# Kernel tuning notes

Hardware: AMD Instinct MI355X
Metric: run time of the kernel (lower is better)

The kernel has to match this reference:

```python
import jax, jax.numpy as jnp
import numpy as np
from jax import lax

BN_EPS = 1e-5


def fps(xyz, n_group):
    """Farthest point sampling. xyz: (B,N,3) -> indices (B,n_group)."""
    B, N, _ = xyz.shape

    def step(carry, _):
        dist, far = carry                                   # (B,N), (B,)
        c = jnp.take_along_axis(xyz, far[:, None, None], axis=1)  # (B,1,3)
        d = jnp.sum((xyz - c) ** 2, axis=-1)                # (B,N)
        dist = jnp.minimum(dist, d)
        return (dist, jnp.argmax(dist, axis=-1).astype(jnp.int32)), far

    init = (jnp.full((B, N), 1e10, xyz.dtype), jnp.zeros((B,), jnp.int32))
    _, idxs = lax.scan(step, init, None, length=n_group)
    return jnp.swapaxes(idxs, 0, 1)                         # (B,n_group)


def knn_point(k, xyz, center):
    """k nearest neighbors of each center in xyz. -> idx (B,G,k)."""
    # squared distances (B,G,N), expanded-cdist form
    d = (jnp.sum(center ** 2, -1)[:, :, None]
         + jnp.sum(xyz ** 2, -1)[:, None, :]
         - 2.0 * jnp.einsum('bgc,bnc->bgn', center, xyz))
    _, idx = lax.top_k(-d, k)                               # smallest distances
    return idx


def batchnorm(x, gamma, beta):
    """Training-mode BatchNorm1d over (M, n) per channel. x: (M,n,C)."""
    mu = jnp.mean(x, axis=(0, 1))
    var = jnp.var(x, axis=(0, 1))
    return (x - mu) * lax.rsqrt(var + BN_EPS) * gamma + beta


def encoder(pg, W1, b1, g1, be1, W2, b2, W3, b3, g2, be2, W4, b4):
    """PointNet encoder. pg: (B,G,n,3) -> (B,G,C)."""
    B, G, n, _ = pg.shape
    x = pg.reshape(B * G, n, 3)
    f = jnp.einsum('mnc,oc->mno', x, W1) + b1               # (M,n,128)
    f = jax.nn.relu(batchnorm(f, g1, be1))
    f = jnp.einsum('mnc,oc->mno', f, W2) + b2               # (M,n,256)
    fg = jnp.max(f, axis=1, keepdims=True)                  # (M,1,256)
    f = jnp.concatenate([jnp.broadcast_to(fg, f.shape), f], axis=-1)  # (M,n,512)
    f = jnp.einsum('mnc,oc->mno', f, W3) + b3               # (M,n,512)
    f = jax.nn.relu(batchnorm(f, g2, be2))
    f = jnp.einsum('mnc,oc->mno', f, W4) + b4               # (M,n,C)
    return jnp.max(f, axis=1).reshape(B, G, -1)


def setup_inputs() -> dict:
    key = jax.random.key(0)
    ks = jax.random.split(key, 8)
    C = 128
    xyz = jax.random.normal(ks[0], (16, 8192, 3), jnp.float32)
    s = 0.02
    return {
        'xyz': xyz,
        'W1': jax.random.normal(ks[1], (128, 3), jnp.float32) * s,
        'b1': jnp.zeros((128,), jnp.float32),
        'g1': jnp.ones((128,), jnp.float32),
        'be1': jnp.zeros((128,), jnp.float32),
        'W2': jax.random.normal(ks[2], (256, 128), jnp.float32) * s,
        'b2': jnp.zeros((256,), jnp.float32),
        'W3': jax.random.normal(ks[3], (512, 512), jnp.float32) * s,
        'b3': jnp.zeros((512,), jnp.float32),
        'g2': jnp.ones((512,), jnp.float32),
        'be2': jnp.zeros((512,), jnp.float32),
        'W4': jax.random.normal(ks[4], (C, 512), jnp.float32) * s,
        'b4': jnp.zeros((C,), jnp.float32),
        'n_group': 512,
    }


def reference(xyz, W1, b1, g1, be1, W2, b2, W3, b3, g2, be2, W4, b4, n_group):
    k = 32
    B, N, _ = xyz.shape
    cidx = fps(xyz, n_group)                                # (B,G)
    center = jnp.take_along_axis(xyz, cidx[:, :, None], axis=1)  # (B,G,3)
    idx = knn_point(k, xyz, center)                         # (B,G,k)
    # gather neighborhoods
    neighborhood = jnp.take_along_axis(
        xyz, idx.reshape(B, n_group * k)[:, :, None], axis=1
    ).reshape(B, n_group, k, 3)
    features = encoder(neighborhood, W1, b1, g1, be1, W2, b2, W3, b3, g2, be2, W4, b4)
    return center, features
```

## Files before the change

kernel.cpp:

```cpp
#include <hip/hip_runtime.h>

typedef unsigned short ushortT;
typedef unsigned int uintT;
typedef unsigned long long u64T;
typedef __bf16 bf16x8 __attribute__((ext_vector_type(8)));
typedef float f32x4 __attribute__((ext_vector_type(4)));

#define B_ 16
#define N_ 8192
#define G_ 512
#define KNN_ 32
#define M_ (B_*G_)
#define R_ (M_*KNN_)

static __device__ __forceinline__ ushortT f2bf(float f){
  uintT u = __float_as_uint(f);
  return (ushortT)((u + 0x7fffu + ((u >> 16) & 1u)) >> 16);
}
static __device__ __forceinline__ float bf2f(ushortT h){ return __uint_as_float(((uintT)h) << 16); }

union U16 { uint4 u; ushortT s[8]; bf16x8 v; };

__global__ __launch_bounds__(1024) void fps_kernel(const float* __restrict__ xyz,
                                                   float* __restrict__ center){
  const int b = blockIdx.x;
  const int tid = threadIdx.x;
  const float* P = xyz + (size_t)b * N_ * 3;
  __shared__ float sx[N_], sy[N_], sz[N_];
  __shared__ u64T slot[2][16];
  float px[8], py[8], pz[8], dist[8];
  uintT nI[8];
#pragma unroll
  for (int k = 0; k < 8; k++){
    int p = tid + (k << 10);
    float x = P[p*3+0], y = P[p*3+1], z = P[p*3+2];
    sx[p] = x; sy[p] = y; sz[p] = z;
    px[k] = x; py[k] = y; pz[k] = z;
    dist[k] = 1e10f;
    nI[k] = ~(uintT)p;
  }
  __syncthreads();
  const int lane = tid & 63, wid = tid >> 6;
  int far = 0;
  for (int s = 0; s < G_; s++){
    const float cx = sx[far], cy = sy[far], cz = sz[far];
    if (tid == 0){
      float* co = center + ((size_t)b * G_ + s) * 3;
      co[0] = cx; co[1] = cy; co[2] = cz;
    }
    u64T best = 0ull;
#pragma unroll
    for (int k = 0; k < 8; k++){
      float d0 = __fsub_rn(px[k], cx), d1 = __fsub_rn(py[k], cy), d2 = __fsub_rn(pz[k], cz);
      float d  = __fadd_rn(__fadd_rn(__fmul_rn(d0,d0), __fmul_rn(d1,d1)), __fmul_rn(d2,d2));
      float dd = fminf(dist[k], d);
      dist[k] = dd;
      u64T pk = ((u64T)__float_as_uint(dd) << 32) | nI[k];
      best = (pk > best) ? pk : best;
    }
#pragma unroll
    for (int m = 32; m >= 1; m >>= 1){
      u64T o = __shfl_xor(best, m);
      best = (o > best) ? o : best;
    }
    if (lane == 0) slot[s & 1][wid] = best;
    __syncthreads();
    u64T v = slot[s & 1][lane & 15];
#pragma unroll
    for (int m = 8; m >= 1; m >>= 1){
      u64T o = __shfl_xor(v, m);
      v = (o > v) ? o : v;
    }
    far = (int)(~(uintT)v);
  }
}

__global__ __launch_bounds__(256) void knn_kernel(const float* __restrict__ xyz,
                                                  const float* __restrict__ center,
                                                  int* __restrict__ knnIdx){
  const int mc = blockIdx.x;
  const int b  = mc >> 9;
  const int tid = threadIdx.x;
  const int lane = tid & 63, w = tid >> 6;
  const float* P = xyz + (size_t)b * N_ * 3;
  const float cx = center[mc*3+0], cy = center[mc*3+1], cz = center[mc*3+2];
  const float tc = __fadd_rn(__fadd_rn(__fmul_rn(cx,cx), __fmul_rn(cy,cy)), __fmul_rn(cz,cz));
  uintT key[32];
  uintT bd = 0xFFFFFFFFu; int bk = 0;
#pragma unroll
  for (int k = 0; k < 32; k++){
    int p = tid + (k << 8);
    float x = P[p*3+0], y = P[p*3+1], z = P[p*3+2];
    float tx  = __fadd_rn(__fadd_rn(__fmul_rn(x,x), __fmul_rn(y,y)), __fmul_rn(z,z));
    float dot = __fadd_rn(__fadd_rn(__fmul_rn(cx,x), __fmul_rn(cy,y)), __fmul_rn(cz,z));
    float d   = __fsub_rn(__fadd_rn(tc, tx), __fmul_rn(2.0f, dot));
    uintT bb  = __float_as_uint(d);
    uintT kk  = bb ^ ((uintT)((int)bb >> 31) | 0x80000000u);
    key[k] = kk;
    if (kk < bd){ bd = kk; bk = k; }
  }
  __shared__ u64T sKeys[128];
  for (int r = 0; r < KNN_; r++){
    u64T me = ((u64T)bd << 32) | (uintT)(tid + (bk << 8));
    u64T m = me;
#pragma unroll
    for (int msk = 32; msk >= 1; msk >>= 1){
      u64T o = __shfl_xor(m, msk);
      m = (o < m) ? o : m;
    }
    if (lane == 0) sKeys[w * 32 + r] = m;
    if (me == m){
      uintT nb = 0xFFFFFFFFu; int nk = 0;
#pragma unroll
      for (int k = 0; k < 32; k++){
        uintT vv = (k == bk) ? 0xFFFFFFFFu : key[k];
        key[k] = vv;
        if (vv < nb){ nb = vv; nk = k; }
      }
      bd = nb; bk = nk;
    }
  }
  __syncthreads();
  if (w == 0){
    u64T e0 = sKeys[lane], e1 = sKeys[lane + 64];
    for (int r = 0; r < KNN_; r++){
      u64T be = (e0 < e1) ? e0 : e1;
      u64T m = be;
#pragma unroll
      for (int msk = 32; msk >= 1; msk >>= 1){
        u64T o = __shfl_xor(m, msk);
        m = (o < m) ? o : m;
      }
      if (lane == 0) knnIdx[(size_t)mc * KNN_ + r] = (int)(uintT)m;
      if (be == m){
        if (e0 == m) e0 = ~0ull; else e1 = ~0ull;
      }
    }
  }
}

__global__ __launch_bounds__(256) void moments_kernel(const float* __restrict__ xyz,
                                                      const int* __restrict__ knnIdx,
                                                      float* __restrict__ Mpart){
  const int t = threadIdx.x, blk = blockIdx.x;
  float m[9];
#pragma unroll
  for (int k = 0; k < 9; k++) m[k] = 0.f;
  for (int i = 0; i < 4; i++){
    int row = blk * 1024 + i * 256 + t;
    int p = knnIdx[row];
    int b = row >> 14;
    const float* pt = xyz + ((size_t)(b * N_ + p)) * 3;
    float x = pt[0], y = pt[1], z = pt[2];
    m[0]+=x; m[1]+=y; m[2]+=z; m[3]+=x*x; m[4]+=y*y; m[5]+=z*z; m[6]+=x*y; m[7]+=x*z; m[8]+=y*z;
  }
  __shared__ float red[4][9];
  const int lane = t & 63, w = t >> 6;
#pragma unroll
  for (int k = 0; k < 9; k++){
    float v = m[k];
#pragma unroll
    for (int sh = 32; sh >= 1; sh >>= 1) v += __shfl_xor(v, sh);
    if (lane == 0) red[w][k] = v;
  }
  __syncthreads();
  if (t < 9) Mpart[blk * 9 + t] = red[0][t] + red[1][t] + red[2][t] + red[3][t];
}

__global__ __launch_bounds__(128) void prep1_kernel(const float* __restrict__ Mpart,
                                                    const float* __restrict__ W1,
                                                    const float* __restrict__ b1,
                                                    const float* __restrict__ g1,
                                                    const float* __restrict__ be1,
                                                    float4* __restrict__ F1c){
  __shared__ float S[9];
  const int t = threadIdx.x;
  if (t < 9){
    float s = 0.f;
    for (int i = 0; i < 256; i++) s += Mpart[i * 9 + t];
    S[t] = s;
  }
  __syncthreads();
  const float invN = 1.0f / (float)R_;
  float mx = S[0]*invN, my = S[1]*invN, mz = S[2]*invN;
  float Cxx = S[3]*invN - mx*mx, Cyy = S[4]*invN - my*my, Czz = S[5]*invN - mz*mz;
  float Cxy = S[6]*invN - mx*my, Cxz = S[7]*invN - mx*mz, Cyz = S[8]*invN - my*mz;
  const int ch = t;
  float w0 = W1[ch*3+0], w1 = W1[ch*3+1], w2 = W1[ch*3+2], bb = b1[ch];
  float var = w0*w0*Cxx + w1*w1*Cyy + w2*w2*Czz + 2.f*(w0*w1*Cxy + w0*w2*Cxz + w1*w2*Cyz);
  float mu  = w0*mx + w1*my + w2*mz + bb;
  float sc  = rsqrtf(var + 1e-5f) * g1[ch];
  float sh  = be1[ch] - mu * sc;
  F1c[ch] = make_float4(w0*sc, w1*sc, w2*sc, fmaf(bb, sc, sh));
}

__global__ __launch_bounds__(256) void cast3_kernel(const float* __restrict__ W2,
                                                    const float* __restrict__ W3,
                                                    const float* __restrict__ W4,
                                                    ushortT* W2b, ushortT* W3b, ushortT* W4b){
  int i = blockIdx.x * 256 + threadIdx.x;
  if (i < 32768)  W2b[i] = f2bf(W2[i]);
  if (i < 262144) W3b[i] = f2bf(W3[i]);
  if (i < 65536)  W4b[i] = f2bf(W4[i]);
}

static __device__ __forceinline__ void a1_frags(const float* __restrict__ xyz,
                                                const int* __restrict__ knnIdx,
                                                const float4* __restrict__ F1c,
                                                int row, int lg, bf16x8 fr[4]){
  const int p = knnIdx[row];
  const int b = row >> 14;
  const float* pt = xyz + ((size_t)(b * N_ + p)) * 3;
  const float x = pt[0], y = pt[1], z = pt[2];
#pragma unroll
  for (int s = 0; s < 4; s++){
    U16 u;
#pragma unroll
    for (int j = 0; j < 8; j++){
      const float4 f = F1c[s * 32 + lg * 8 + j];
      const float h = fmaxf(fmaf(x, f.x, fmaf(y, f.y, fmaf(z, f.z, f.w))), 0.f);
      u.s[j] = f2bf(h);
    }
    fr[s] = u.v;
  }
}

__global__ __launch_bounds__(256) void f2g_kernel(const float* __restrict__ xyz,
                                                  const int* __restrict__ knnIdx,
                                                  const float4* __restrict__ F1c,
                                                  const ushortT* __restrict__ W2bf,
                                                  const float* __restrict__ b2,
                                                  ushortT* __restrict__ fg){
  const int rc = blockIdx.x;
  const int t = threadIdx.x, lane = t & 63, w = t >> 6;
  const int lr = lane & 15, lg = lane >> 4;
  const int row = rc * 64 + w * 16 + lr;
  bf16x8 a1[4];
  a1_frags(xyz, knnIdx, F1c, row, lg, a1);
  f32x4 acc[16];
#pragma unroll
  for (int c = 0; c < 16; c++) acc[c] = (f32x4){0.f,0.f,0.f,0.f};
#pragma unroll
  for (int s = 0; s < 4; s++)
#pragma unroll
    for (int ct = 0; ct < 16; ct++){
      bf16x8 bb = *reinterpret_cast<const bf16x8*>(W2bf + (size_t)(ct*16+lr)*128 + s*32 + lg*8);
      acc[ct] = __builtin_amdgcn_mfma_f32_16x16x32_bf16(a1[s], bb, acc[ct], 0, 0, 0);
    }
  __shared__ float wmax[4][256];
#pragma unroll
  for (int ct = 0; ct < 16; ct++){
    float cmax = fmaxf(fmaxf(acc[ct][0], acc[ct][1]), fmaxf(acc[ct][2], acc[ct][3]));
    cmax = fmaxf(cmax, __shfl_xor(cmax, 16));
    cmax = fmaxf(cmax, __shfl_xor(cmax, 32));
    if (lg == 0) wmax[w][ct*16+lr] = cmax;
  }
  __syncthreads();
  {
    float bb = b2[t];
    fg[((size_t)rc*2 + 0)*256 + t] = f2bf(fmaxf(wmax[0][t], wmax[1][t]) + bb);
    fg[((size_t)rc*2 + 1)*256 + t] = f2bf(fmaxf(wmax[2][t], wmax[3][t]) + bb);
  }
}

__global__ __launch_bounds__(256) void u_kernel(const ushortT* __restrict__ fg,
                                                const ushortT* __restrict__ W3bf,
                                                const float* __restrict__ b3,
                                                float* __restrict__ U){
  const int bid = blockIdx.x;
  const int rc = bid >> 2, cc = bid & 3;
  const int t = threadIdx.x, lane = t & 63, w = t >> 6;
  const int lr = lane & 15, lg = lane >> 4;
  const int arow = rc * 64 + w * 16 + lr;
  f32x4 acc[8];
#pragma unroll
  for (int c = 0; c < 8; c++) acc[c] = (f32x4){0.f,0.f,0.f,0.f};
#pragma unroll
  for (int s = 0; s < 8; s++){
    bf16x8 a = *reinterpret_cast<const bf16x8*>(fg + (size_t)arow*256 + s*32 + lg*8);
#pragma unroll
    for (int ct = 0; ct < 8; ct++){
      bf16x8 bb = *reinterpret_cast<const bf16x8*>(W3bf + (size_t)(cc*128+ct*16+lr)*512 + s*32 + lg*8);
      acc[ct] = __builtin_amdgcn_mfma_f32_16x16x32_bf16(a, bb, acc[ct], 0, 0, 0);
    }
  }
#pragma unroll
  for (int ct = 0; ct < 8; ct++){
    int col = cc*128 + ct*16 + lr;
    float bb = b3[col];
#pragma unroll
    for (int i = 0; i < 4; i++){
      int crow = rc*64 + w*16 + lg*4 + i;
      U[(size_t)crow * 512 + col] = acc[ct][i] + bb;
    }
  }
}

static __device__ __forceinline__ void phaseA_s2(const float* __restrict__ xyz,
                                                 const int* __restrict__ knnIdx,
                                                 const float4* __restrict__ F1c,
                                                 const ushortT* __restrict__ W2bf,
                                                 const float* __restrict__ b2,
                                                 ushortT* sS2, int blk,
                                                 int wv, int lr, int lg){
  bf16x8 a1[4];
  a1_frags(xyz, knnIdx, F1c, blk*128 + wv*16 + lr, lg, a1);
  f32x4 acc[16];
#pragma unroll
  for (int c = 0; c < 16; c++) acc[c] = (f32x4){0.f,0.f,0.f,0.f};
#pragma unroll
  for (int s = 0; s < 4; s++)
#pragma unroll
    for (int ct = 0; ct < 16; ct++){
      bf16x8 bb = *reinterpret_cast<const bf16x8*>(W2bf + (size_t)(ct*16+lr)*128 + s*32 + lg*8);
      acc[ct] = __builtin_amdgcn_mfma_f32_16x16x32_bf16(a1[s], bb, acc[ct], 0, 0, 0);
    }
#pragma unroll
  for (int ct = 0; ct < 16; ct++){
    int col = ct*16 + lr;
    float bb = b2[col];
#pragma unroll
    for (int i = 0; i < 4; i++){
      int row = wv*16 + lg*4 + i;
      sS2[row*256 + (col ^ ((row & 7) << 3))] = f2bf(acc[ct][i] + bb);
    }
  }
}

#define PHASE2(PASS, ACC)                                                               \
  {                                                                                     \
    _Pragma("unroll")                                                                   \
    for (int s = 0; s < 8; s++){                                                        \
      const int kk = s*32 + lg*8;                                                       \
      bf16x8 b0 = *reinterpret_cast<const bf16x8*>(                                     \
          W3bf + (size_t)((PASS)*256 + wv*32 + 0 + lr)*512 + 256 + kk);                 \
      bf16x8 b1 = *reinterpret_cast<const bf16x8*>(                                     \
          W3bf + (size_t)((PASS)*256 + wv*32 + 16 + lr)*512 + 256 + kk);                \
      _Pragma("unroll")                                                                 \
      for (int rf = 0; rf < 8; rf++){                                                   \
        int row = rf*16 + lr;                                                           \
        bf16x8 a = *reinterpret_cast<const bf16x8*>(                                    \
            &sS2[row*256 + (kk ^ ((row & 7) << 3))]);                                   \
        ACC[rf][0] = __builtin_amdgcn_mfma_f32_16x16x32_bf16(a, b0, ACC[rf][0], 0,0,0); \
        ACC[rf][1] = __builtin_amdgcn_mfma_f32_16x16x32_bf16(a, b1, ACC[rf][1], 0,0,0); \
      }                                                                                 \
    }                                                                                   \
  }

__global__ __launch_bounds__(512) void enc3_kernel(const float* __restrict__ xyz,
                                                   const int* __restrict__ knnIdx,
                                                   const float4* __restrict__ F1c,
                                                   const ushortT* __restrict__ W2bf,
                                                   const float* __restrict__ b2,
                                                   const ushortT* __restrict__ W3bf,
                                                   const float* __restrict__ U,
                                                   float* __restrict__ P2sum,
                                                   float* __restrict__ P2sq){
  __shared__ ushortT sS2[128 * 256];
  const int blk = blockIdx.x;
  const int t = threadIdx.x, lane = t & 63, wv = t >> 6;
  const int lr = lane & 15, lg = lane >> 4;
  phaseA_s2(xyz, knnIdx, F1c, W2bf, b2, sS2, blk, wv, lr, lg);
  __syncthreads();
#pragma unroll
  for (int pass = 0; pass < 2; pass++){
    f32x4 acc[8][2];
#pragma unroll
    for (int rf = 0; rf < 8; rf++){ acc[rf][0] = (f32x4){0,0,0,0}; acc[rf][1] = (f32x4){0,0,0,0}; }
    PHASE2(pass, acc)
#pragma unroll
    for (int ct = 0; ct < 2; ct++){
      int col = pass*256 + wv*32 + ct*16 + lr;
      float s = 0.f, q = 0.f;
#pragma unroll
      for (int rf = 0; rf < 8; rf++){
        float uv = U[(size_t)(blk*4 + (rf >> 1)) * 512 + col];
#pragma unroll
        for (int i = 0; i < 4; i++){
          float v = acc[rf][ct][i] + uv;
          s += v; q += v * v;
        }
      }
      s += __shfl_xor(s, 16); s += __shfl_xor(s, 32);
      q += __shfl_xor(q, 16); q += __shfl_xor(q, 32);
      if (lg == 0){
        P2sum[(size_t)blk * 512 + col] = s;
        P2sq [(size_t)blk * 512 + col] = q;
      }
    }
  }
}

__global__ __launch_bounds__(256) void fin_kernel(const float* __restrict__ Psum,
                                                  const float* __restrict__ Psq,
                                                  int nPart, int C, float invN,
                                                  const float* __restrict__ g,
                                                  const float* __restrict__ be,
                                                  float* __restrict__ scale,
                                                  float* __restrict__ shift){
  const int ch = blockIdx.x, t = threadIdx.x;
  float s = 0.f, q = 0.f;
  for (int i = t; i < nPart; i += 256){
    s += Psum[(size_t)i * C + ch];
    q += Psq [(size_t)i * C + ch];
  }
  __shared__ float ls[4], lq[4];
#pragma unroll
  for (int m = 32; m >= 1; m >>= 1){ s += __shfl_xor(s, m); q += __shfl_xor(q, m); }
  if ((t & 63) == 0){ ls[t >> 6] = s; lq[t >> 6] = q; }
  __syncthreads();
  if (t == 0){
    s = ls[0] + ls[1] + ls[2] + ls[3];
    q = lq[0] + lq[1] + lq[2] + lq[3];
    float mu = s * invN;
    float var = q * invN - mu * mu;
    float sc = rsqrtf(var + 1e-5f) * g[ch];
    scale[ch] = sc;
    shift[ch] = be[ch] - mu * sc;
  }
}

__global__ __launch_bounds__(512) void enc4_kernel(const float* __restrict__ xyz,
                                                   const int* __restrict__ knnIdx,
                                                   const float4* __restrict__ F1c,
                                                   const ushortT* __restrict__ W2bf,
                                                   const float* __restrict__ b2,
                                                   const ushortT* __restrict__ W3bf,
                                                   const float* __restrict__ U,
                                                   const float* __restrict__ scale2,
                                                   const float* __restrict__ shift2,
                                                   const ushortT* __restrict__ W4bf,
                                                   const float* __restrict__ b4,
                                                   float* __restrict__ feat){
  __shared__ ushortT sS2[128 * 256];
  __shared__ float s_sc[512], s_sh[512];
  const int blk = blockIdx.x;
  const int t = threadIdx.x, lane = t & 63, wv = t >> 6;
  const int lr = lane & 15, lg = lane >> 4;
  if (t < 512){ s_sc[t] = scale2[t]; s_sh[t] = shift2[t]; }
  phaseA_s2(xyz, knnIdx, F1c, W2bf, b2, sS2, blk, wv, lr, lg);
  __syncthreads();
  f32x4 acc0[8][2], acc1[8][2];
#pragma unroll
  for (int rf = 0; rf < 8; rf++){
    acc0[rf][0] = (f32x4){0,0,0,0}; acc0[rf][1] = (f32x4){0,0,0,0};
    acc1[rf][0] = (f32x4){0,0,0,0}; acc1[rf][1] = (f32x4){0,0,0,0};
  }
  PHASE2(0, acc0)
  PHASE2(1, acc1)
  __syncthreads();
  f32x4 accF[8];
#pragma unroll
  for (int rf = 0; rf < 8; rf++) accF[rf] = (f32x4){0,0,0,0};
#pragma unroll
  for (int ct = 0; ct < 2; ct++){
    int colh = wv*32 + ct*16 + lr;
#pragma unroll
    for (int rf = 0; rf < 8; rf++){
      float uv = U[(size_t)(blk*4 + (rf >> 1)) * 512 + colh];
#pragma unroll
      for (int i = 0; i < 4; i++){
        int row = rf*16 + lg*4 + i;
        float v = acc0[rf][ct][i] + uv;
        sS2[row*256 + (colh ^ ((row & 7) << 3))] =
            f2bf(fmaxf(fmaf(v, s_sc[colh], s_sh[colh]), 0.f));
      }
    }
  }
  __syncthreads();
#pragma unroll
  for (int s = 0; s < 8; s++){
    const int kk = s*32 + lg*8;
    bf16x8 b = *reinterpret_cast<const bf16x8*>(W4bf + (size_t)(wv*16 + lr)*512 + kk);
#pragma unroll
    for (int rf = 0; rf < 8; rf++){
      int row = rf*16 + lr;
      bf16x8 a = *reinterpret_cast<const bf16x8*>(&sS2[row*256 + (kk ^ ((row & 7) << 3))]);
      accF[rf] = __builtin_amdgcn_mfma_f32_16x16x32_bf16(a, b, accF[rf], 0, 0, 0);
    }
  }
  __syncthreads();
#pragma unroll
  for (int ct = 0; ct < 2; ct++){
    int colh = wv*32 + ct*16 + lr;
    int col  = 256 + colh;
#pragma unroll
    for (int rf = 0; rf < 8; rf++){
      float uv = U[(size_t)(blk*4 + (rf >> 1)) * 512 + col];
#pragma unroll
      for (int i = 0; i < 4; i++){
        int row = rf*16 + lg*4 + i;
        float v = acc1[rf][ct][i] + uv;
        sS2[row*256 + (colh ^ ((row & 7) << 3))] =
            f2bf(fmaxf(fmaf(v, s_sc[col], s_sh[col]), 0.f));
      }
    }
  }
  __syncthreads();
#pragma unroll
  for (int s = 0; s < 8; s++){
    const int kk = s*32 + lg*8;
    bf16x8 b = *reinterpret_cast<const bf16x8*>(W4bf + (size_t)(wv*16 + lr)*512 + 256 + kk);
#pragma unroll
    for (int rf = 0; rf < 8; rf++){
      int row = rf*16 + lr;
      bf16x8 a = *reinterpret_cast<const bf16x8*>(&sS2[row*256 + (kk ^ ((row & 7) << 3))]);
      accF[rf] = __builtin_amdgcn_mfma_f32_16x16x32_bf16(a, b, accF[rf], 0, 0, 0);
    }
  }
  const float bb4 = b4[wv*16 + lr];
#pragma unroll
  for (int gl = 0; gl < 4; gl++){
    float m = -3.0e38f;
#pragma unroll
    for (int i = 0; i < 4; i++){
      m = fmaxf(m, accF[2*gl    ][i]);
      m = fmaxf(m, accF[2*gl + 1][i]);
    }
    m = fmaxf(m, __shfl_xor(m, 16));
    m = fmaxf(m, __shfl_xor(m, 32));
    if (lg == 0)
      feat[((size_t)blk*4 + gl)*128 + wv*16 + lr] = m + bb4;
  }
}

extern "C" void kernel_launch(void* const* d_in, const int* in_sizes, int n_in,
                              void* d_out, int out_size, void* d_ws, size_t ws_size,
                              hipStream_t stream){
  const float* xyz = (const float*)d_in[0];
  const float* W1  = (const float*)d_in[1];
  const float* b1  = (const float*)d_in[2];
  const float* g1  = (const float*)d_in[3];
  const float* be1 = (const float*)d_in[4];
  const float* W2  = (const float*)d_in[5];
  const float* b2  = (const float*)d_in[6];
  const float* W3  = (const float*)d_in[7];
  const float* b3  = (const float*)d_in[8];
  const float* g2  = (const float*)d_in[9];
  const float* be2 = (const float*)d_in[10];
  const float* W4  = (const float*)d_in[11];
  const float* b4  = (const float*)d_in[12];

  float* out = (float*)d_out;
  float* center = out;
  float* feat   = out + (size_t)B_ * G_ * 3;

  char* p = (char*)d_ws;
  size_t used = 0;
  auto alloc = [&](size_t bytes) -> char* {
    char* r = p + used; used += (bytes + 255) & ~(size_t)255; return r;
  };
  int*     knnIdx = (int*)    alloc((size_t)R_ * 4);
  ushortT* W2bf   = (ushortT*)alloc(32768 * 2);
  ushortT* W3bf   = (ushortT*)alloc(262144 * 2);
  ushortT* W4bf   = (ushortT*)alloc(65536 * 2);
  float4*  F1c    = (float4*) alloc(128 * 16);
  float*   Mpart  = (float*)  alloc(256 * 9 * 4);
  ushortT* fg     = (ushortT*)alloc((size_t)M_ * 256 * 2);
  float*   U      = (float*)  alloc((size_t)M_ * 512 * 4);
  float*   P2sum  = (float*)  alloc((size_t)2048 * 512 * 4);
  float*   P2sq   = (float*)  alloc((size_t)2048 * 512 * 4);
  float*   scale2 = (float*)  alloc(512 * 4);
  float*   shift2 = (float*)  alloc(512 * 4);

  cast3_kernel  <<<dim3(1024), dim3(256),  0, stream>>>(W2, W3, W4, W2bf, W3bf, W4bf);
  fps_kernel    <<<dim3(B_),   dim3(1024), 0, stream>>>(xyz, center);
  knn_kernel    <<<dim3(M_),   dim3(256),  0, stream>>>(xyz, center, knnIdx);
  moments_kernel<<<dim3(256),  dim3(256),  0, stream>>>(xyz, knnIdx, Mpart);
  prep1_kernel  <<<dim3(1),    dim3(128),  0, stream>>>(Mpart, W1, b1, g1, be1, F1c);
  f2g_kernel    <<<dim3(4096), dim3(256),  0, stream>>>(xyz, knnIdx, F1c, W2bf, b2, fg);
  u_kernel      <<<dim3(512),  dim3(256),  0, stream>>>(fg, W3bf, b3, U);
  enc3_kernel   <<<dim3(2048), dim3(512),  0, stream>>>(xyz, knnIdx, F1c, W2bf, b2, W3bf, U, P2sum, P2sq);
  fin_kernel    <<<dim3(512),  dim3(256),  0, stream>>>(P2sum, P2sq, 2048, 512, 1.0f/(float)R_, g2, be2, scale2, shift2);
  enc4_kernel   <<<dim3(2048), dim3(512),  0, stream>>>(xyz, knnIdx, F1c, W2bf, b2, W3bf, U,
                                                        scale2, shift2, W4bf, b4, feat);
}
```

Before: 1.713 ms.

## Split FPS per batch across four cooperating blocks with global atomic argmax exchange

```diff
diff --git a/kernel.cpp b/kernel.cpp
--- a/kernel.cpp
+++ b/kernel.cpp
@@ -21,41 +21,43 @@
 
 union U16 { uint4 u; ushortT s[8]; bf16x8 v; };
 
-__global__ __launch_bounds__(1024) void fps_kernel(const float* __restrict__ xyz,
-                                                   float* __restrict__ center){
-  const int b = blockIdx.x;
+__global__ __launch_bounds__(512) void fps_kernel(const float* __restrict__ xyz,
+                                                  float* __restrict__ center,
+                                                  u64T* __restrict__ gslot){
+  const int bid = blockIdx.x;
+  const int b = bid >> 2, bq = bid & 3;
   const int tid = threadIdx.x;
+  const int lane = tid & 63, wv = tid >> 6;
   const float* P = xyz + (size_t)b * N_ * 3;
-  __shared__ float sx[N_], sy[N_], sz[N_];
-  __shared__ u64T slot[2][16];
-  float px[8], py[8], pz[8], dist[8];
-  uintT nI[8];
-#pragma unroll
-  for (int k = 0; k < 8; k++){
-    int p = tid + (k << 10);
-    float x = P[p*3+0], y = P[p*3+1], z = P[p*3+2];
-    sx[p] = x; sy[p] = y; sz[p] = z;
-    px[k] = x; py[k] = y; pz[k] = z;
+  const int base = bq * 2048;
+  float px[4], py[4], pz[4], dist[4];
+  uintT tkey[4];
+#pragma unroll
+  for (int k = 0; k < 4; k++){
+    int p = base + tid + (k << 9);
+    px[k] = P[p*3+0]; py[k] = P[p*3+1]; pz[k] = P[p*3+2];
     dist[k] = 1e10f;
-    nI[k] = ~(uintT)p;
-  }
-  __syncthreads();
-  const int lane = tid & 63, wid = tid >> 6;
+    tkey[k] = (uintT)(8191 - p);
+  }
+  __shared__ u64T wslot[8];
+  __shared__ int s_far;
+  u64T* myslots = gslot + (size_t)b * 4 * 8;
   int far = 0;
   for (int s = 0; s < G_; s++){
-    const float cx = sx[far], cy = sy[far], cz = sz[far];
-    if (tid == 0){
+    const int fu = __builtin_amdgcn_readfirstlane(far);
+    const float cx = P[fu*3+0], cy = P[fu*3+1], cz = P[fu*3+2];
+    if (bq == 0 && tid == 0){
       float* co = center + ((size_t)b * G_ + s) * 3;
       co[0] = cx; co[1] = cy; co[2] = cz;
     }
     u64T best = 0ull;
 #pragma unroll
-    for (int k = 0; k < 8; k++){
+    for (int k = 0; k < 4; k++){
       float d0 = __fsub_rn(px[k], cx), d1 = __fsub_rn(py[k], cy), d2 = __fsub_rn(pz[k], cz);
       float d  = __fadd_rn(__fadd_rn(__fmul_rn(d0,d0), __fmul_rn(d1,d1)), __fmul_rn(d2,d2));
       float dd = fminf(dist[k], d);
       dist[k] = dd;
-      u64T pk = ((u64T)__float_as_uint(dd) << 32) | nI[k];
+      u64T pk = ((u64T)__float_as_uint(dd) << 32) | tkey[k];
       best = (pk > best) ? pk : best;
     }
 #pragma unroll
@@ -63,15 +65,33 @@
       u64T o = __shfl_xor(best, m);
       best = (o > best) ? o : best;
     }
-    if (lane == 0) slot[s & 1][wid] = best;
+    if (lane == 0) wslot[wv] = best;
     __syncthreads();
-    u64T v = slot[s & 1][lane & 15];
-#pragma unroll
-    for (int m = 8; m >= 1; m >>= 1){
-      u64T o = __shfl_xor(v, m);
-      v = (o > v) ? o : v;
-    }
-    far = (int)(~(uintT)v);
+    if (wv == 0){
+      u64T v = wslot[lane & 7];
+#pragma unroll
+      for (int m = 4; m >= 1; m >>= 1){
+        u64T o = __shfl_xor(v, m);
+        v = (o > v) ? o : v;
+      }
+      if (lane == 0){
+        u64T pub = ((u64T)(s + 1) << 54) | ((v >> 32) << 22) | (v & 0x1FFFull);
+        __hip_atomic_store(&myslots[bq * 8], pub, __ATOMIC_RELEASE, __HIP_MEMORY_SCOPE_AGENT);
+      }
+      u64T got = 0ull;
+      if (lane < 4){
+        const u64T want = (u64T)(s + 1);
+        int guard = 0;
+        do {
+          got = __hip_atomic_load(&myslots[lane * 8], __ATOMIC_ACQUIRE, __HIP_MEMORY_SCOPE_AGENT);
+        } while ((got >> 54) != want && ++guard < (1 << 20));
+      }
+      u64T g1 = __shfl_xor(got, 1); got = (g1 > got) ? g1 : got;
+      u64T g2 = __shfl_xor(got, 2); got = (g2 > got) ? g2 : got;
+      if (lane == 0) s_far = 8191 - (int)(got & 0x1FFFull);
+    }
+    __syncthreads();
+    far = s_far;
   }
 }
 
@@ -551,6 +571,7 @@
     char* r = p + used; used += (bytes + 255) & ~(size_t)255; return r;
   };
   int*     knnIdx = (int*)    alloc((size_t)R_ * 4);
+  u64T*    gslot  = (u64T*)   alloc((size_t)B_ * 4 * 8 * 8);
   ushortT* W2bf   = (ushortT*)alloc(32768 * 2);
   ushortT* W3bf   = (ushortT*)alloc(262144 * 2);
   ushortT* W4bf   = (ushortT*)alloc(65536 * 2);
@@ -564,7 +585,7 @@
   float*   shift2 = (float*)  alloc(512 * 4);
 
   cast3_kernel  <<<dim3(1024), dim3(256),  0, stream>>>(W2, W3, W4, W2bf, W3bf, W4bf);
-  fps_kernel    <<<dim3(B_),   dim3(1024), 0, stream>>>(xyz, center);
+  fps_kernel    <<<dim3(B_*4), dim3(512),  0, stream>>>(xyz, center, gslot);
   knn_kernel    <<<dim3(M_),   dim3(256),  0, stream>>>(xyz, center, knnIdx);
   moments_kernel<<<dim3(256),  dim3(256),  0, stream>>>(xyz, knnIdx, Mpart);
   prep1_kernel  <<<dim3(1),    dim3(128),  0, stream>>>(Mpart, W1, b1, g1, be1, F1c);
```

Measured after the change: 2.185 ms. 27.6% more time.

## Compute second BatchNorm statistics via Gram matrix instead of full layer-3 pass

Applied to the files above, without the earlier changes.

```diff
diff --git a/kernel.cpp b/kernel.cpp
--- a/kernel.cpp
+++ b/kernel.cpp
@@ -225,12 +225,13 @@
   }
 }
 
-__global__ __launch_bounds__(256) void f2g_kernel(const float* __restrict__ xyz,
-                                                  const int* __restrict__ knnIdx,
-                                                  const float4* __restrict__ F1c,
-                                                  const ushortT* __restrict__ W2bf,
-                                                  const float* __restrict__ b2,
-                                                  ushortT* __restrict__ fg){
+__global__ __launch_bounds__(256) void f2g2_kernel(const float* __restrict__ xyz,
+                                                   const int* __restrict__ knnIdx,
+                                                   const float4* __restrict__ F1c,
+                                                   const ushortT* __restrict__ W2bf,
+                                                   const float* __restrict__ b2,
+                                                   ushortT* __restrict__ fg,
+                                                   float* __restrict__ fgsum){
   const int rc = blockIdx.x;
   const int t = threadIdx.x, lane = t & 63, w = t >> 6;
   const int lr = lane & 15, lg = lane >> 4;
@@ -248,18 +249,27 @@
       acc[ct] = __builtin_amdgcn_mfma_f32_16x16x32_bf16(a1[s], bb, acc[ct], 0, 0, 0);
     }
   __shared__ float wmax[4][256];
+  __shared__ float wsum[4][256];
 #pragma unroll
   for (int ct = 0; ct < 16; ct++){
+    float bb = b2[ct*16 + lr];
     float cmax = fmaxf(fmaxf(acc[ct][0], acc[ct][1]), fmaxf(acc[ct][2], acc[ct][3]));
+    float csum = 0.f;
+#pragma unroll
+    for (int i = 0; i < 4; i++)
+      csum += bf2f(f2bf(acc[ct][i] + bb));
     cmax = fmaxf(cmax, __shfl_xor(cmax, 16));
     cmax = fmaxf(cmax, __shfl_xor(cmax, 32));
-    if (lg == 0) wmax[w][ct*16+lr] = cmax;
+    csum += __shfl_xor(csum, 16); csum += __shfl_xor(csum, 32);
+    if (lg == 0){ wmax[w][ct*16+lr] = cmax; wsum[w][ct*16+lr] = csum; }
   }
   __syncthreads();
   {
     float bb = b2[t];
     fg[((size_t)rc*2 + 0)*256 + t] = f2bf(fmaxf(wmax[0][t], wmax[1][t]) + bb);
     fg[((size_t)rc*2 + 1)*256 + t] = f2bf(fmaxf(wmax[2][t], wmax[3][t]) + bb);
+    fgsum[((size_t)rc*2 + 0)*256 + t] = wsum[0][t] + wsum[1][t];
+    fgsum[((size_t)rc*2 + 1)*256 + t] = wsum[2][t] + wsum[3][t];
   }
 }
 
@@ -293,6 +303,228 @@
       int crow = rc*64 + w*16 + lg*4 + i;
       U[(size_t)crow * 512 + col] = acc[ct][i] + bb;
     }
+  }
+}
+
+__global__ __launch_bounds__(256) void v_kernel(const float* __restrict__ fgsum,
+                                                const ushortT* __restrict__ W3bf,
+                                                const float* __restrict__ U,
+                                                float* __restrict__ UVpart){
+  const int bid = blockIdx.x;
+  const int rc = bid >> 2, cc = bid & 3;
+  const int t = threadIdx.x, lane = t & 63, w = t >> 6;
+  const int lr = lane & 15, lg = lane >> 4;
+  const int arow = rc * 64 + w * 16 + lr;
+  f32x4 acc[8];
+#pragma unroll
+  for (int c = 0; c < 8; c++) acc[c] = (f32x4){0.f,0.f,0.f,0.f};
+#pragma unroll
+  for (int s = 0; s < 8; s++){
+    int kk = s*32 + lg*8;
+    float4 fa = *reinterpret_cast<const float4*>(&fgsum[(size_t)arow*256 + kk]);
+    float4 fb = *reinterpret_cast<const float4*>(&fgsum[(size_t)arow*256 + kk + 4]);
+    U16 ua;
+    ua.s[0]=f2bf(fa.x); ua.s[1]=f2bf(fa.y); ua.s[2]=f2bf(fa.z); ua.s[3]=f2bf(fa.w);
+    ua.s[4]=f2bf(fb.x); ua.s[5]=f2bf(fb.y); ua.s[6]=f2bf(fb.z); ua.s[7]=f2bf(fb.w);
+#pragma unroll
+    for (int ct = 0; ct < 8; ct++){
+      bf16x8 bb = *reinterpret_cast<const bf16x8*>(W3bf + (size_t)(cc*128+ct*16+lr)*512 + 256 + kk);
+      acc[ct] = __builtin_amdgcn_mfma_f32_16x16x32_bf16(ua.v, bb, acc[ct], 0, 0, 0);
+    }
+  }
+  __shared__ float sUV[4][128];
+#pragma unroll
+  for (int ct = 0; ct < 8; ct++){
+    int col = cc*128 + ct*16 + lr;
+    float uv = 0.f;
+#pragma unroll
+    for (int i = 0; i < 4; i++){
+      int g = rc*64 + w*16 + lg*4 + i;
+      uv += acc[ct][i] * U[(size_t)g * 512 + col];
+    }
+    uv += __shfl_xor(uv, 16); uv += __shfl_xor(uv, 32);
+    if (lg == 0) sUV[w][ct*16+lr] = uv;
+  }
+  __syncthreads();
+  if (t < 128)
+    UVpart[(size_t)rc * 512 + cc*128 + t] = sUV[0][t] + sUV[1][t] + sUV[2][t] + sUV[3][t];
+}
+
+__global__ __launch_bounds__(512) void gram_kernel(const float* __restrict__ xyz,
+                                                   const int* __restrict__ knnIdx,
+                                                   const float4* __restrict__ F1c,
+                                                   const ushortT* __restrict__ W2bf,
+                                                   const float* __restrict__ b2,
+                                                   float* __restrict__ Gpart,
+                                                   int tilesPerBlk){
+  __shared__ ushortT sT[256 * 128];
+  const int blk = blockIdx.x;
+  const int t = threadIdx.x, lane = t & 63, wv = t >> 6;
+  const int lr = lane & 15, lg = lane >> 4;
+  f32x4 gacc[32];
+#pragma unroll
+  for (int c = 0; c < 32; c++) gacc[c] = (f32x4){0.f,0.f,0.f,0.f};
+  for (int tile = 0; tile < tilesPerBlk; tile++){
+    const int rt = blk * tilesPerBlk + tile;
+    bf16x8 a1[4];
+    a1_frags(xyz, knnIdx, F1c, rt*128 + wv*16 + lr, lg, a1);
+    f32x4 acc[16];
+#pragma unroll
+    for (int c = 0; c < 16; c++) acc[c] = (f32x4){0.f,0.f,0.f,0.f};
+#pragma unroll
+    for (int s = 0; s < 4; s++)
+#pragma unroll
+      for (int ct = 0; ct < 16; ct++){
+        bf16x8 bb = *reinterpret_cast<const bf16x8*>(W2bf + (size_t)(ct*16+lr)*128 + s*32 + lg*8);
+        acc[ct] = __builtin_amdgcn_mfma_f32_16x16x32_bf16(a1[s], bb, acc[ct], 0, 0, 0);
+      }
+    __syncthreads();
+#pragma unroll
+    for (int ct = 0; ct < 16; ct++){
+      int col = ct*16 + lr;
+      float bb = b2[col];
+#pragma unroll
+      for (int i = 0; i < 4; i++){
+        int row = wv*16 + lg*4 + i;
+        sT[col*128 + (row ^ ((col & 7) << 3))] = f2bf(acc[ct][i] + bb);
+      }
+    }
+    __syncthreads();
+#pragma unroll
+    for (int ks = 0; ks < 4; ks++){
+      const int k0 = ks*32 + lg*8;
+      bf16x8 aA[2];
+#pragma unroll
+      for (int ii = 0; ii < 2; ii++){
+        int c = (2*wv + ii)*16 + lr;
+        aA[ii] = *reinterpret_cast<const bf16x8*>(&sT[c*128 + (k0 ^ ((c & 7) << 3))]);
+      }
+#pragma unroll
+      for (int j = 0; j < 16; j++){
+        int c = j*16 + lr;
+        bf16x8 bB = *reinterpret_cast<const bf16x8*>(&sT[c*128 + (k0 ^ ((c & 7) << 3))]);
+        gacc[0*16+j] = __builtin_amdgcn_mfma_f32_16x16x32_bf16(aA[0], bB, gacc[0*16+j], 0,0,0);
+        gacc[1*16+j] = __builtin_amdgcn_mfma_f32_16x16x32_bf16(aA[1], bB, gacc[1*16+j], 0,0,0);
+      }
+    }
+  }
+  float* Gp = Gpart + (size_t)blk * 65536;
+#pragma unroll
+  for (int ii = 0; ii < 2; ii++)
+#pragma unroll
+    for (int j = 0; j < 16; j++)
+#pragma unroll
+      for (int i = 0; i < 4; i++){
+        int ci = (2*wv + ii)*16 + lg*4 + i;
+        int cj = j*16 + lr;
+        Gp[ci*256 + cj] = gacc[ii*16+j][i];
+      }
+}
+
+__global__ __launch_bounds__(256) void gred_kernel(const float* __restrict__ Gpart,
+                                                   float* __restrict__ G, int nPart){
+  int i = blockIdx.x * 256 + threadIdx.x;
+  float s = 0.f;
+  for (int b = 0; b < nPart; b++) s += Gpart[(size_t)b * 65536 + i];
+  G[i] = s;
+}
+
+__global__ __launch_bounds__(256) void ured_kernel(const float* __restrict__ U,
+                                                   const float* __restrict__ fgsum,
+                                                   float* __restrict__ Upart,
+                                                   float* __restrict__ Usqpart,
+                                                   float* __restrict__ CSpart){
+  const int blk = blockIdx.x;
+  const int slice = blk >> 3, part = blk & 7;
+  const int t = threadIdx.x;
+  {
+    const int cl = t & 63, gsub = t >> 6;
+    const int c = part*64 + cl;
+    float su = 0.f, sq = 0.f;
+    for (int g = slice*1024 + gsub; g < slice*1024 + 1024; g += 4){
+      float u = U[(size_t)g * 512 + c];
+      su += u; sq += u*u;
+    }
+    __shared__ float rU[4][64], rQ[4][64];
+    rU[gsub][cl] = su; rQ[gsub][cl] = sq;
+    __syncthreads();
+    if (t < 64){
+      Upart  [(size_t)slice*512 + part*64 + t] = rU[0][t]+rU[1][t]+rU[2][t]+rU[3][t];
+      Usqpart[(size_t)slice*512 + part*64 + t] = rQ[0][t]+rQ[1][t]+rQ[2][t]+rQ[3][t];
+    }
+  }
+  __syncthreads();
+  {
+    const int cl = t & 31, gsub = t >> 5;
+    const int c2 = part*32 + cl;
+    float cs = 0.f;
+    for (int g = slice*1024 + gsub; g < slice*1024 + 1024; g += 8)
+      cs += fgsum[(size_t)g * 256 + c2];
+    __shared__ float rC[8][32];
+    rC[gsub][cl] = cs;
+    __syncthreads();
+    if (t < 32){
+      float s = 0.f;
+#pragma unroll
+      for (int k = 0; k < 8; k++) s += rC[k][t];
+      CSpart[(size_t)slice*256 + part*32 + t] = s;
+    }
+  }
+}
+
+__global__ __launch_bounds__(256) void fin2_kernel(const float* __restrict__ G,
+                                                   const float* __restrict__ CSpart,
+                                                   const float* __restrict__ Upart,
+                                                   const float* __restrict__ Usqpart,
+                                                   const float* __restrict__ UVpart,
+                                                   const ushortT* __restrict__ W3bf,
+                                                   const float* __restrict__ g2,
+                                                   const float* __restrict__ be2,
+                                                   float* __restrict__ scale2,
+                                                   float* __restrict__ shift2){
+  const int blk = blockIdx.x, t = threadIdx.x;
+  __shared__ float sw[256];
+  __shared__ float r1[4], r2[4], r3[4];
+  float csf = 0.f;
+#pragma unroll
+  for (int s = 0; s < 8; s++) csf += CSpart[s*256 + t];
+  for (int sub = 0; sub < 4; sub++){
+    const int c = blk*4 + sub;
+    sw[t] = bf2f(W3bf[(size_t)c*512 + 256 + t]);
+    __syncthreads();
+    const float wj = sw[t];
+    float dot = 0.f;
+    const float* Grow = G + (size_t)t * 256;
+    for (int k = 0; k < 256; k++) dot += sw[k] * Grow[k];
+    float quad = wj * dot;
+    float cdot = wj * csf;
+    float uvv  = (t < 128) ? UVpart[(size_t)t * 512 + c] : 0.f;
+    float a = quad, bq = cdot, cq = uvv;
+#pragma unroll
+    for (int m = 32; m >= 1; m >>= 1){
+      a  += __shfl_xor(a, m); bq += __shfl_xor(bq, m); cq += __shfl_xor(cq, m);
+    }
+    if ((t & 63) == 0){ r1[t>>6] = a; r2[t>>6] = bq; r3[t>>6] = cq; }
+    __syncthreads();
+    if (t == 0){
+      float wGw  = r1[0]+r1[1]+r1[2]+r1[3];
+      float csw  = r2[0]+r2[1]+r2[2]+r2[3];
+      float sUV  = r3[0]+r3[1]+r3[2]+r3[3];
+      float sU = 0.f, sQ = 0.f;
+#pragma unroll
+      for (int s = 0; s < 8; s++){
+        sU += Upart  [s*512 + c];
+        sQ += Usqpart[s*512 + c];
+      }
+      const float invN = 1.0f / (float)R_;
+      float mu = (csw + 32.f * sU) * invN;
+      float e2 = (wGw + 2.f * sUV + 32.f * sQ) * invN;
+      float var = e2 - mu * mu;
+      float sc = rsqrtf(var + 1e-5f) * g2[c];
+      scale2[c] = sc;
+      shift2[c] = be2[c] - mu * sc;
+    }
+    __syncthreads();
   }
 }
 
@@ -557,21 +789,47 @@
   float4*  F1c    = (float4*) alloc(128 * 16);
   float*   Mpart  = (float*)  alloc(256 * 9 * 4);
   ushortT* fg     = (ushortT*)alloc((size_t)M_ * 256 * 2);
+  float*   fgsum  = (float*)  alloc((size_t)M_ * 256 * 4);
   float*   U      = (float*)  alloc((size_t)M_ * 512 * 4);
-  float*   P2sum  = (float*)  alloc((size_t)2048 * 512 * 4);
-  float*   P2sq   = (float*)  alloc((size_t)2048 * 512 * 4);
   float*   scale2 = (float*)  alloc(512 * 4);
   float*   shift2 = (float*)  alloc(512 * 4);
+
+  const size_t uvp_b  = (size_t)128 * 512 * 4;
+  const size_t g_b    = (size_t)65536 * 4;
+  const size_t small_b= (size_t)(8*512*4)*2 + (size_t)8*256*4;
+  const size_t margin = 1 << 20;
+  int NB = 0;
+  if      (ws_size >= used + uvp_b + g_b + small_b + (size_t)128*65536*4 + margin) NB = 128;
+  else if (ws_size >= used + uvp_b + g_b + small_b + (size_t)64 *65536*4 + margin) NB = 64;
 
   cast3_kernel  <<<dim3(1024), dim3(256),  0, stream>>>(W2, W3, W4, W2bf, W3bf, W4bf);
   fps_kernel    <<<dim3(B_),   dim3(1024), 0, stream>>>(xyz, center);
   knn_kernel    <<<dim3(M_),   dim3(256),  0, stream>>>(xyz, center, knnIdx);
   moments_kernel<<<dim3(256),  dim3(256),  0, stream>>>(xyz, knnIdx, Mpart);
   prep1_kernel  <<<dim3(1),    dim3(128),  0, stream>>>(Mpart, W1, b1, g1, be1, F1c);
-  f2g_kernel    <<<dim3(4096), dim3(256),  0, stream>>>(xyz, knnIdx, F1c, W2bf, b2, fg);
+  f2g2_kernel   <<<dim3(4096), dim3(256),  0, stream>>>(xyz, knnIdx, F1c, W2bf, b2, fg, fgsum);
   u_kernel      <<<dim3(512),  dim3(256),  0, stream>>>(fg, W3bf, b3, U);
-  enc3_kernel   <<<dim3(2048), dim3(512),  0, stream>>>(xyz, knnIdx, F1c, W2bf, b2, W3bf, U, P2sum, P2sq);
-  fin_kernel    <<<dim3(512),  dim3(256),  0, stream>>>(P2sum, P2sq, 2048, 512, 1.0f/(float)R_, g2, be2, scale2, shift2);
-  enc4_kernel   <<<dim3(2048), dim3(512),  0, stream>>>(xyz, knnIdx, F1c, W2bf, b2, W3bf, U,
-                                                        scale2, shift2, W4bf, b4, feat);
-}
+
+  if (NB){
+    float* UVpart  = (float*)alloc(uvp_b);
+    float* Gpart   = (float*)alloc((size_t)NB * 65536 * 4);
+    float* G       = (float*)alloc(g_b);
+    float* Upart   = (float*)alloc(8 * 512 * 4);
+    float* Usqpart = (float*)alloc(8 * 512 * 4);
+    float* CSpart  = (float*)alloc(8 * 256 * 4);
+    v_kernel   <<<dim3(512), dim3(256), 0, stream>>>(fgsum, W3bf, U, UVpart);
+    gram_kernel<<<dim3(NB),  dim3(512), 0, stream>>>(xyz, knnIdx, F1c, W2bf, b2, Gpart, 2048/NB);
+    gred_kernel<<<dim3(256), dim3(256), 0, stream>>>(Gpart, G, NB);
+    ured_kernel<<<dim3(64),  dim3(256), 0, stream>>>(U, fgsum, Upart, Usqpart, CSpart);
+    fin2_kernel<<<dim3(128), dim3(256), 0, stream>>>(G, CSpart, Upart, Usqpart, UVpart,
+                                                     W3bf, g2, be2, scale2, shift2);
+  } else {
+    float* P2sum = (float*)alloc((size_t)2048 * 512 * 4);
+    float* P2sq  = (float*)alloc((size_t)2048 * 512 * 4);
+    enc3_kernel<<<dim3(2048), dim3(512), 0, stream>>>(xyz, knnIdx, F1c, W2bf, b2, W3bf, U, P2sum, P2sq);
+    fin_kernel <<<dim3(512),  dim3(256), 0, stream>>>(P2sum, P2sq, 2048, 512, 1.0f/(float)R_,
+                                                      g2, be2, scale2, shift2);
+  }
+  enc4_kernel  <<<dim3(2048), dim3(512), 0, stream>>>(xyz, knnIdx, F1c, W2bf, b2, W3bf, U,
+                                                      scale2, shift2, W4bf, b4, feat);
+}
```

Result: slower. 2.450 ms (+43.0%).

## Fuse FPS and KNN into one persistent kernel with flag-based producer/consumer overlap

Applied to the files above, without the earlier changes.

```diff
diff --git a/kernel.cpp b/kernel.cpp
--- a/kernel.cpp
+++ b/kernel.cpp
@@ -12,6 +12,7 @@
 #define KNN_ 32
 #define M_ (B_*G_)
 #define R_ (M_*KNN_)
+#define FLAG_TAG 0x5EED0000
 
 static __device__ __forceinline__ ushortT f2bf(float f){
   uintT u = __float_as_uint(f);
@@ -21,120 +22,148 @@
 
 union U16 { uint4 u; ushortT s[8]; bf16x8 v; };
 
-__global__ __launch_bounds__(1024) void fps_kernel(const float* __restrict__ xyz,
-                                                   float* __restrict__ center){
-  const int b = blockIdx.x;
-  const int tid = threadIdx.x;
-  const float* P = xyz + (size_t)b * N_ * 3;
+__global__ __launch_bounds__(256) void clearflags_kernel(int* __restrict__ flags){
+  flags[blockIdx.x * 256 + threadIdx.x] = 0;
+}
+
+__global__ __launch_bounds__(1024) void fps_knn_kernel(const float* __restrict__ xyz,
+                                                       float* __restrict__ center,
+                                                       int* __restrict__ flags,
+                                                       int* __restrict__ knnIdx){
   __shared__ float sx[N_], sy[N_], sz[N_];
   __shared__ u64T slot[2][16];
-  float px[8], py[8], pz[8], dist[8];
-  uintT nI[8];
-#pragma unroll
-  for (int k = 0; k < 8; k++){
-    int p = tid + (k << 10);
-    float x = P[p*3+0], y = P[p*3+1], z = P[p*3+2];
-    sx[p] = x; sy[p] = y; sz[p] = z;
-    px[k] = x; py[k] = y; pz[k] = z;
-    dist[k] = 1e10f;
-    nI[k] = ~(uintT)p;
-  }
-  __syncthreads();
-  const int lane = tid & 63, wid = tid >> 6;
-  int far = 0;
-  for (int s = 0; s < G_; s++){
-    const float cx = sx[far], cy = sy[far], cz = sz[far];
-    if (tid == 0){
-      float* co = center + ((size_t)b * G_ + s) * 3;
-      co[0] = cx; co[1] = cy; co[2] = cz;
-    }
-    u64T best = 0ull;
+  __shared__ u64T wcand[16 * 32];
+  __shared__ float s_c[3];
+  const int bid = blockIdx.x;
+  const int tid = threadIdx.x;
+  const int lane = tid & 63, wv = tid >> 6;
+
+  if (bid < B_){
+    const int b = bid;
+    const float* P = xyz + (size_t)b * N_ * 3;
+    float px[8], py[8], pz[8], dist[8];
 #pragma unroll
     for (int k = 0; k < 8; k++){
-      float d0 = __fsub_rn(px[k], cx), d1 = __fsub_rn(py[k], cy), d2 = __fsub_rn(pz[k], cz);
-      float d  = __fadd_rn(__fadd_rn(__fmul_rn(d0,d0), __fmul_rn(d1,d1)), __fmul_rn(d2,d2));
-      float dd = fminf(dist[k], d);
-      dist[k] = dd;
-      u64T pk = ((u64T)__float_as_uint(dd) << 32) | nI[k];
-      best = (pk > best) ? pk : best;
-    }
-#pragma unroll
-    for (int m = 32; m >= 1; m >>= 1){
-      u64T o = __shfl_xor(best, m);
-      best = (o > best) ? o : best;
-    }
-    if (lane == 0) slot[s & 1][wid] = best;
+      int p = tid + (k << 10);
+      float x = P[p*3+0], y = P[p*3+1], z = P[p*3+2];
+      sx[p] = x; sy[p] = y; sz[p] = z;
+      px[k] = x; py[k] = y; pz[k] = z;
+      dist[k] = 1e10f;
+    }
     __syncthreads();
-    u64T v = slot[s & 1][lane & 15];
-#pragma unroll
-    for (int m = 8; m >= 1; m >>= 1){
-      u64T o = __shfl_xor(v, m);
-      v = (o > v) ? o : v;
-    }
-    far = (int)(~(uintT)v);
-  }
-}
-
-__global__ __launch_bounds__(256) void knn_kernel(const float* __restrict__ xyz,
-                                                  const float* __restrict__ center,
-                                                  int* __restrict__ knnIdx){
-  const int mc = blockIdx.x;
-  const int b  = mc >> 9;
-  const int tid = threadIdx.x;
-  const int lane = tid & 63, w = tid >> 6;
-  const float* P = xyz + (size_t)b * N_ * 3;
-  const float cx = center[mc*3+0], cy = center[mc*3+1], cz = center[mc*3+2];
-  const float tc = __fadd_rn(__fadd_rn(__fmul_rn(cx,cx), __fmul_rn(cy,cy)), __fmul_rn(cz,cz));
-  uintT key[32];
-  uintT bd = 0xFFFFFFFFu; int bk = 0;
-#pragma unroll
-  for (int k = 0; k < 32; k++){
-    int p = tid + (k << 8);
-    float x = P[p*3+0], y = P[p*3+1], z = P[p*3+2];
-    float tx  = __fadd_rn(__fadd_rn(__fmul_rn(x,x), __fmul_rn(y,y)), __fmul_rn(z,z));
-    float dot = __fadd_rn(__fadd_rn(__fmul_rn(cx,x), __fmul_rn(cy,y)), __fmul_rn(cz,z));
-    float d   = __fsub_rn(__fadd_rn(tc, tx), __fmul_rn(2.0f, dot));
-    uintT bb  = __float_as_uint(d);
-    uintT kk  = bb ^ ((uintT)((int)bb >> 31) | 0x80000000u);
-    key[k] = kk;
-    if (kk < bd){ bd = kk; bk = k; }
-  }
-  __shared__ u64T sKeys[128];
-  for (int r = 0; r < KNN_; r++){
-    u64T me = ((u64T)bd << 32) | (uintT)(tid + (bk << 8));
-    u64T m = me;
-#pragma unroll
-    for (int msk = 32; msk >= 1; msk >>= 1){
-      u64T o = __shfl_xor(m, msk);
-      m = (o < m) ? o : m;
-    }
-    if (lane == 0) sKeys[w * 32 + r] = m;
-    if (me == m){
-      uintT nb = 0xFFFFFFFFu; int nk = 0;
-#pragma unroll
-      for (int k = 0; k < 32; k++){
-        uintT vv = (k == bk) ? 0xFFFFFFFFu : key[k];
-        key[k] = vv;
-        if (vv < nb){ nb = vv; nk = k; }
-      }
-      bd = nb; bk = nk;
-    }
-  }
-  __syncthreads();
-  if (w == 0){
-    u64T e0 = sKeys[lane], e1 = sKeys[lane + 64];
-    for (int r = 0; r < KNN_; r++){
-      u64T be = (e0 < e1) ? e0 : e1;
-      u64T m = be;
-#pragma unroll
-      for (int msk = 32; msk >= 1; msk >>= 1){
-        u64T o = __shfl_xor(m, msk);
-        m = (o < m) ? o : m;
-      }
-      if (lane == 0) knnIdx[(size_t)mc * KNN_ + r] = (int)(uintT)m;
-      if (be == m){
-        if (e0 == m) e0 = ~0ull; else e1 = ~0ull;
-      }
+    int far = 0;
+    for (int s = 0; s < G_; s++){
+      const float cx = sx[far], cy = sy[far], cz = sz[far];
+      if (tid == 0){
+        float* co = center + ((size_t)b * G_ + s) * 3;
+        co[0] = cx; co[1] = cy; co[2] = cz;
+        __hip_atomic_store(&flags[b * G_ + s], FLAG_TAG + s,
+                           __ATOMIC_RELEASE, __HIP_MEMORY_SCOPE_AGENT);
+      }
+      float bv = -1.0f; int bi = 0;
+#pragma unroll
+      for (int k = 0; k < 8; k++){
+        float d0 = __fsub_rn(px[k], cx), d1 = __fsub_rn(py[k], cy), d2 = __fsub_rn(pz[k], cz);
+        float d  = __fadd_rn(__fadd_rn(__fmul_rn(d0,d0), __fmul_rn(d1,d1)), __fmul_rn(d2,d2));
+        float dd = fminf(dist[k], d);
+        dist[k] = dd;
+        if (dd > bv){ bv = dd; bi = tid + (k << 10); }
+      }
+      u64T best = ((u64T)__float_as_uint(bv) << 32) | (uintT)(~bi);
+#pragma unroll
+      for (int m = 32; m >= 1; m >>= 1){
+        u64T o = __shfl_xor(best, m);
+        best = (o > best) ? o : best;
+      }
+      if (lane == 0) slot[s & 1][wv] = best;
+      __syncthreads();
+      u64T v = slot[s & 1][lane & 15];
+#pragma unroll
+      for (int m = 8; m >= 1; m >>= 1){
+        u64T o = __shfl_xor(v, m);
+        v = (o > v) ? o : v;
+      }
+      far = (int)(~(uintT)v) & (N_ - 1);
+    }
+  } else {
+    const int idx = bid - B_;
+    const int b = idx / 15;
+    const int j = idx % 15;
+    const float* P = xyz + (size_t)b * N_ * 3;
+#pragma unroll
+    for (int k = 0; k < 8; k++){
+      int p = tid + (k << 10);
+      sx[p] = P[p*3+0]; sy[p] = P[p*3+1]; sz[p] = P[p*3+2];
+    }
+    __syncthreads();
+    for (int s = j; s < G_; s += 15){
+      if (tid == 0){
+        const int want = FLAG_TAG + s;
+        int guard = 0;
+        while (__hip_atomic_load(&flags[b * G_ + s],
+                                 __ATOMIC_ACQUIRE, __HIP_MEMORY_SCOPE_AGENT) != want
+               && ++guard < (1 << 24)) {}
+        const float* cp = center + ((size_t)b * G_ + s) * 3;
+        s_c[0] = __hip_atomic_load(cp + 0, __ATOMIC_RELAXED, __HIP_MEMORY_SCOPE_AGENT);
+        s_c[1] = __hip_atomic_load(cp + 1, __ATOMIC_RELAXED, __HIP_MEMORY_SCOPE_AGENT);
+        s_c[2] = __hip_atomic_load(cp + 2, __ATOMIC_RELAXED, __HIP_MEMORY_SCOPE_AGENT);
+      }
+      __syncthreads();
+      const float cx = s_c[0], cy = s_c[1], cz = s_c[2];
+      const float tc = __fadd_rn(__fadd_rn(__fmul_rn(cx,cx), __fmul_rn(cy,cy)), __fmul_rn(cz,cz));
+      uintT key[8];
+      uintT bd = 0xFFFFFFFFu; int bk = 0;
+#pragma unroll
+      for (int k = 0; k < 8; k++){
+        int p = tid + (k << 10);
+        float x = sx[p], y = sy[p], z = sz[p];
+        float tx  = __fadd_rn(__fadd_rn(__fmul_rn(x,x), __fmul_rn(y,y)), __fmul_rn(z,z));
+        float dot = __fadd_rn(__fadd_rn(__fmul_rn(cx,x), __fmul_rn(cy,y)), __fmul_rn(cz,z));
+        float d   = __fsub_rn(__fadd_rn(tc, tx), __fmul_rn(2.0f, dot));
+        uintT bb  = __float_as_uint(d);
+        uintT kk  = bb ^ ((uintT)((int)bb >> 31) | 0x80000000u);
+        key[k] = kk;
+        if (kk < bd){ bd = kk; bk = k; }
+      }
+      for (int r = 0; r < KNN_; r++){
+        u64T me = ((u64T)bd << 32) | (uintT)(tid + (bk << 10));
+        u64T m = me;
+#pragma unroll
+        for (int mk = 32; mk >= 1; mk >>= 1){
+          u64T o = __shfl_xor(m, mk);
+          m = (o < m) ? o : m;
+        }
+        if (lane == 0) wcand[wv * 32 + r] = m;
+        if (me == m){
+          uintT nb = 0xFFFFFFFFu; int nk = 0;
+#pragma unroll
+          for (int k = 0; k < 8; k++){
+            uintT vv = (k == bk) ? 0xFFFFFFFFu : key[k];
+            key[k] = vv;
+            if (vv < nb){ nb = vv; nk = k; }
+          }
+          bd = nb; bk = nk;
+        }
+      }
+      __syncthreads();
+      if (wv == 0){
+        int pos = 0;
+        u64T head = (lane < 16) ? wcand[lane * 32] : ~0ull;
+        for (int r = 0; r < KNN_; r++){
+          u64T m = head;
+#pragma unroll
+          for (int mk = 8; mk >= 1; mk >>= 1){
+            u64T o = __shfl_xor(m, mk);
+            m = (o < m) ? o : m;
+          }
+          if (lane == 0) knnIdx[(size_t)(b * G_ + s) * KNN_ + r] = (int)(uintT)m;
+          if (lane < 16 && head == m){
+            pos++;
+            head = (pos < 32) ? wcand[lane * 32 + pos] : ~0ull;
+          }
+        }
+      }
+      __syncthreads();
     }
   }
 }
@@ -551,6 +580,7 @@
     char* r = p + used; used += (bytes + 255) & ~(size_t)255; return r;
   };
   int*     knnIdx = (int*)    alloc((size_t)R_ * 4);
+  int*     flags  = (int*)    alloc((size_t)M_ * 4);
   ushortT* W2bf   = (ushortT*)alloc(32768 * 2);
   ushortT* W3bf   = (ushortT*)alloc(262144 * 2);
   ushortT* W4bf   = (ushortT*)alloc(65536 * 2);
@@ -563,15 +593,16 @@
   float*   scale2 = (float*)  alloc(512 * 4);
   float*   shift2 = (float*)  alloc(512 * 4);
 
-  cast3_kernel  <<<dim3(1024), dim3(256),  0, stream>>>(W2, W3, W4, W2bf, W3bf, W4bf);
-  fps_kernel    <<<dim3(B_),   dim3(1024), 0, stream>>>(xyz, center);
-  knn_kernel    <<<dim3(M_),   dim3(256),  0, stream>>>(xyz, center, knnIdx);
-  moments_kernel<<<dim3(256),  dim3(256),  0, stream>>>(xyz, knnIdx, Mpart);
-  prep1_kernel  <<<dim3(1),    dim3(128),  0, stream>>>(Mpart, W1, b1, g1, be1, F1c);
-  f2g_kernel    <<<dim3(4096), dim3(256),  0, stream>>>(xyz, knnIdx, F1c, W2bf, b2, fg);
-  u_kernel      <<<dim3(512),  dim3(256),  0, stream>>>(fg, W3bf, b3, U);
-  enc3_kernel   <<<dim3(2048), dim3(512),  0, stream>>>(xyz, knnIdx, F1c, W2bf, b2, W3bf, U, P2sum, P2sq);
-  fin_kernel    <<<dim3(512),  dim3(256),  0, stream>>>(P2sum, P2sq, 2048, 512, 1.0f/(float)R_, g2, be2, scale2, shift2);
-  enc4_kernel   <<<dim3(2048), dim3(512),  0, stream>>>(xyz, knnIdx, F1c, W2bf, b2, W3bf, U,
-                                                        scale2, shift2, W4bf, b4, feat);
-}
+  clearflags_kernel<<<dim3(32),  dim3(256),  0, stream>>>(flags);
+  cast3_kernel     <<<dim3(1024),dim3(256),  0, stream>>>(W2, W3, W4, W2bf, W3bf, W4bf);
+  fps_knn_kernel   <<<dim3(256), dim3(1024), 0, stream>>>(xyz, center, flags, knnIdx);
+  moments_kernel   <<<dim3(256), dim3(256),  0, stream>>>(xyz, knnIdx, Mpart);
+  prep1_kernel     <<<dim3(1),   dim3(128),  0, stream>>>(Mpart, W1, b1, g1, be1, F1c);
+  f2g_kernel       <<<dim3(4096),dim3(256),  0, stream>>>(xyz, knnIdx, F1c, W2bf, b2, fg);
+  u_kernel         <<<dim3(512), dim3(256),  0, stream>>>(fg, W3bf, b3, U);
+  enc3_kernel      <<<dim3(2048),dim3(512),  0, stream>>>(xyz, knnIdx, F1c, W2bf, b2, W3bf, U, P2sum, P2sq);
+  fin_kernel       <<<dim3(512), dim3(256),  0, stream>>>(P2sum, P2sq, 2048, 512, 1.0f/(float)R_,
+                                                          g2, be2, scale2, shift2);
+  enc4_kernel      <<<dim3(2048),dim3(512),  0, stream>>>(xyz, knnIdx, F1c, W2bf, b2, W3bf, U,
+                                                          scale2, shift2, W4bf, b4, feat);
+}
```

Result: slower. 1.813 ms (+5.8%).
